# Kernel optimization log

Hardware: AMD Instinct MI355X
Metric: run time of the kernel (lower is better)

## Reference

```python
import jax, jax.numpy as jnp
import numpy as np
import math

DIM = 2048
B = 4
L = 4096
LOCAL_WINDOW = 512
GLOBAL_STRIDE = 1024
TOTAL_SEEN = 65536


def _sparse_cache_positions(total_seen):
    # Positions kept by _build_sparse_cache: local window tail + global strided.
    local_start = max(0, total_seen - LOCAL_WINDOW)
    glob = np.arange(0, local_start, GLOBAL_STRIDE)
    loc = np.arange(local_start, total_seen)
    return np.concatenate([glob, loc]).astype(np.int64)  # sorted, 576 entries


def setup_inputs() -> dict:
    key = jax.random.key(0)
    ks = jax.random.split(key, 12)
    pos = _sparse_cache_positions(TOTAL_SEEN)
    Kc = pos.shape[0]  # 576
    inp = {
        "chunk": jax.random.normal(ks[0], (B, L, DIM), dtype=jnp.float32),
        "cached_k": jax.random.normal(ks[1], (B, Kc, DIM), dtype=jnp.float32),
        "cached_v": jax.random.normal(ks[2], (B, Kc, DIM), dtype=jnp.float32),
        "cached_positions": jnp.asarray(pos),
        "total_seen": TOTAL_SEEN,
        "Wq": jax.random.normal(ks[3], (DIM, DIM), dtype=jnp.float32) * 0.02,
        "bq": jnp.zeros((DIM,), dtype=jnp.float32),
        "Wk": jax.random.normal(ks[4], (DIM, DIM), dtype=jnp.float32) * 0.02,
        "bk": jnp.zeros((DIM,), dtype=jnp.float32),
        "Wv": jax.random.normal(ks[5], (DIM, DIM), dtype=jnp.float32) * 0.02,
        "bv": jnp.zeros((DIM,), dtype=jnp.float32),
        "Wo": jax.random.normal(ks[6], (DIM, DIM), dtype=jnp.float32) * 0.02,
        "bo": jnp.zeros((DIM,), dtype=jnp.float32),
    }
    return inp


def reference(chunk, cached_k, cached_v, cached_positions, total_seen,
              Wq, bq, Wk, bk, Wv, bv, Wo, bo):
    Bn, Ln, D = chunk.shape
    scale = 1.0 / math.sqrt(D)
    # QKV projections (nn.Linear: x @ W.T + b)
    q = chunk @ Wq.T + bq            # [B, L, D]
    new_k = chunk @ Wk.T + bk        # [B, L, D]
    new_v = chunk @ Wv.T + bv
    new_pos = jnp.arange(total_seen, total_seen + Ln)  # [L]
    full_k = jnp.concatenate([cached_k, new_k], axis=1)   # [B, Kc+L, D]
    full_v = jnp.concatenate([cached_v, new_v], axis=1)
    full_pos = jnp.concatenate([cached_positions, new_pos], axis=0)  # [Kc+L]
    # Masked dense attention (causal on absolute positions)
    scores = jnp.einsum('bqd,bkd->bqk', q, full_k) * scale  # [B, L, Kc+L]
    causal = full_pos[None, :] > new_pos[:, None]           # [L, Kc+L]
    scores = jnp.where(causal[None, :, :], -jnp.inf, scores)
    weights = jax.nn.softmax(scores, axis=-1)
    attended = jnp.einsum('bqk,bkd->bqd', weights, full_v)  # [B, L, D]
    return attended @ Wo.T + bo
```

## Files before the change

kernel.cpp:

```cpp
#include <hip/hip_runtime.h>
#include <hip/hip_bf16.h>
#include <hip/hip_fp16.h>
#include <math.h>

#define B_   4
#define L_   4096
#define D_   2048
#define KC_  576
#define KT_  4672
#define KTP_ 4864

typedef __attribute__((ext_vector_type(8))) short short8;
typedef __attribute__((ext_vector_type(4))) float floatx4;

enum { EPI_BF16 = 0, EPI_KV = 1, EPI_SCORE = 2, EPI_F32 = 3 };
enum { FLAG_SWZ = 1, FLAG_KCAP = 2 };

__device__ static inline void gl_lds16(const void* g, void* l) {
  __builtin_amdgcn_global_load_lds((const __attribute__((address_space(1))) void*)g,
                                   (__attribute__((address_space(3))) void*)l,
                                   16, 0, 0);
}

__device__ static inline void barx() {
  asm volatile("" ::: "memory");
  __builtin_amdgcn_s_barrier();
  asm volatile("" ::: "memory");
}

__global__ __launch_bounds__(512, 2) void gemm_bt(
    const ushort* __restrict__ A, int lda,
    const ushort* __restrict__ Bt, int ldb,
    void* __restrict__ out, int ldo,
    const float* __restrict__ bias,
    int K, int mode, int flags, float scale)
{
  __shared__ __align__(16) char smem[2 * 4 * 16384];

  const int t = threadIdx.x;
  const int l = t & 63;
  const int wv = t >> 6;

  int m_idx, n_idx;
  if (flags & FLAG_SWZ) {
    const int total = gridDim.x * gridDim.y;
    const int chunk = total >> 3;
    const int orig = blockIdx.y * gridDim.x + blockIdx.x;
    const int wg = (orig & 7) * chunk + (orig >> 3);
    m_idx = wg % gridDim.y;
    n_idx = wg / gridDim.y;
  } else {
    n_idx = blockIdx.x;
    m_idx = blockIdx.y;
  }
  const int bm = m_idx * 256;
  const int bn = n_idx * 256;

  if (mode == EPI_SCORE && bn >= KC_ + bm + 256) return;
  if (flags & FLAG_KCAP) {
    const int kcap = 832 + 256 * m_idx;
    if (K > kcap) K = kcap;
  }

  const int wr = wv >> 2, wc = wv & 3;
  const int wm = wr << 7;
  const int wcn = wc << 6;
  const int fr = l & 15, fq = l >> 4;
  const int swz = fq ^ ((l >> 1) & 3);

  int offA[8], offB[4];
#pragma unroll
  for (int i = 0; i < 8; ++i) offA[i] = (wm + i * 16 + fr) * 64 + swz * 16;
#pragma unroll
  for (int j = 0; j < 4; ++j) offB[j] = (wcn + j * 16 + fr) * 64 + swz * 16;

  const int srow = t >> 2;
  const int sslot = (t & 3) ^ ((t >> 3) & 3);
  const ushort* Ag = A + (size_t)(bm + srow) * lda + sslot * 8;
  const ushort* Bg = Bt + (size_t)(bn + srow) * ldb + sslot * 8;
  const int wofs = wv << 10;

  auto stageA = [&](int d, int kh, int kt) {
    char* dst = smem + (((d << 2) + kh) << 14) + wofs;
    const ushort* g = Ag + kt + (kh << 5);
    gl_lds16(g, dst);
    gl_lds16(g + ((size_t)lda << 7), dst + 8192);
  };
  auto stageB = [&](int d, int kh, int kt) {
    char* dst = smem + (((d << 2) + 2 + kh) << 14) + wofs;
    const ushort* g = Bg + kt + (kh << 5);
    gl_lds16(g, dst);
    gl_lds16(g + ((size_t)ldb << 7), dst + 8192);
  };

  floatx4 acc[8][4];
#pragma unroll
  for (int i = 0; i < 8; ++i)
#pragma unroll
    for (int j = 0; j < 4; ++j) acc[i][j] = (floatx4)(0.0f);

  const int nkt = K >> 6;
  const int k1 = (nkt > 1) ? 64 : 0;

  stageA(0, 0, 0); stageB(0, 0, 0);
  stageA(0, 1, 0); stageB(0, 1, 0);
  stageA(1, 0, k1); stageB(1, 0, k1);
  asm volatile("s_waitcnt vmcnt(4)" ::: "memory");
  barx();

  for (int T = 0; T < nkt; ++T) {
    const int cur = T & 1;
    const char* rb = smem + (cur << 16);
    const int kA = ((T + 1 < nkt) ? T + 1 : nkt - 1) << 6;
    const int kB = ((T + 2 < nkt) ? T + 2 : nkt - 1) << 6;
    short8 afr[4], bfr[4];

#pragma unroll
    for (int i = 0; i < 4; ++i) afr[i] = *(const short8*)(rb + offA[i]);
#pragma unroll
    for (int j = 0; j < 4; ++j) bfr[j] = *(const short8*)(rb + 32768 + offB[j]);
    stageA(cur ^ 1, 1, kA);
    barx();
    __builtin_amdgcn_s_setprio(1);
#pragma unroll
    for (int i = 0; i < 4; ++i)
#pragma unroll
      for (int j = 0; j < 4; ++j)
        acc[i][j] = __builtin_amdgcn_mfma_f32_16x16x32_bf16(afr[i], bfr[j], acc[i][j], 0, 0, 0);
    __builtin_amdgcn_s_setprio(0);
    barx();

#pragma unroll
    for (int i = 0; i < 4; ++i) afr[i] = *(const short8*)(rb + offA[4 + i]);
    stageB(cur ^ 1, 1, kA);
    barx();
    __builtin_amdgcn_s_setprio(1);
#pragma unroll
    for (int i = 0; i < 4; ++i)
#pragma unroll
      for (int j = 0; j < 4; ++j)
        acc[4 + i][j] = __builtin_amdgcn_mfma_f32_16x16x32_bf16(afr[i], bfr[j], acc[4 + i][j], 0, 0, 0);
    __builtin_amdgcn_s_setprio(0);
    barx();

#pragma unroll
    for (int i = 0; i < 4; ++i) afr[i] = *(const short8*)(rb + 16384 + offA[i]);
#pragma unroll
    for (int j = 0; j < 4; ++j) bfr[j] = *(const short8*)(rb + 49152 + offB[j]);
    stageA(cur, 0, kB);
    barx();
    __builtin_amdgcn_s_setprio(1);
#pragma unroll
    for (int i = 0; i < 4; ++i)
#pragma unroll
      for (int j = 0; j < 4; ++j)
        acc[i][j] = __builtin_amdgcn_mfma_f32_16x16x32_bf16(afr[i], bfr[j], acc[i][j], 0, 0, 0);
    __builtin_amdgcn_s_setprio(0);
    barx();

#pragma unroll
    for (int i = 0; i < 4; ++i) afr[i] = *(const short8*)(rb + 16384 + offA[4 + i]);
    stageB(cur, 0, kB);
    asm volatile("s_waitcnt vmcnt(4)" ::: "memory");
    barx();
    __builtin_amdgcn_s_setprio(1);
#pragma unroll
    for (int i = 0; i < 4; ++i)
#pragma unroll
      for (int j = 0; j < 4; ++j)
        acc[4 + i][j] = __builtin_amdgcn_mfma_f32_16x16x32_bf16(afr[i], bfr[j], acc[4 + i][j], 0, 0, 0);
    __builtin_amdgcn_s_setprio(0);
    barx();
  }

#pragma unroll
  for (int mf = 0; mf < 8; ++mf) {
#pragma unroll
    for (int nf = 0; nf < 4; ++nf) {
      const int col = bn + wcn + nf * 16 + fr;
#pragma unroll
      for (int r = 0; r < 4; ++r) {
        const int row = bm + wm + mf * 16 + fq * 4 + r;
        float v = acc[mf][nf][r];
        if (mode == EPI_SCORE) {
          v *= scale;
          bool masked = (col >= KT_) || (col >= KC_ && (col - KC_) > row);
          if (masked) v = -65504.0f;
          ((__half*)out)[(size_t)row * ldo + col] = __float2half(v);
        } else if (mode == EPI_F32) {
          if (bias) v += bias[col];
          ((float*)out)[(size_t)row * ldo + col] = v;
        } else if (mode == EPI_KV) {
          if (bias) v += bias[col];
          const int b = row >> 12;
          const int ll = row & 4095;
          ((__hip_bfloat16*)out)[((size_t)b * KTP_ + KC_ + ll) * D_ + col] = __float2bfloat16(v);
        } else {
          if (bias) v += bias[col];
          ((__hip_bfloat16*)out)[(size_t)row * ldo + col] = __float2bfloat16(v);
        }
      }
    }
  }
}

__global__ __launch_bounds__(256) void cvt_f32_bf16(const float* __restrict__ in,
                                                    __hip_bfloat16* __restrict__ out, int n) {
  int i = blockIdx.x * 256 + threadIdx.x;
  int stride = gridDim.x * 256;
  for (; i < n; i += stride) out[i] = __float2bfloat16(in[i]);
}

__global__ __launch_bounds__(256) void cvt_weights(const float* __restrict__ wq,
                                                   const float* __restrict__ wk,
                                                   const float* __restrict__ wv,
                                                   const float* __restrict__ wo,
                                                   __hip_bfloat16* __restrict__ out) {
  const int per = D_ * D_;
  const int n = 4 * per;
  int i = blockIdx.x * 256 + threadIdx.x;
  int stride = gridDim.x * 256;
  for (; i < n; i += stride) {
    int w = i / per, rem = i - w * per;
    const float* src = (w == 0) ? wq : (w == 1) ? wk : (w == 2) ? wv : wo;
    out[i] = __float2bfloat16(src[rem]);
  }
}

__global__ __launch_bounds__(256) void cvt_cached(const float* __restrict__ ck,
                                                  const float* __restrict__ cv,
                                                  ushort* __restrict__ fk,
                                                  ushort* __restrict__ fv) {
  const int n = B_ * KC_ * D_;
  int i = blockIdx.x * 256 + threadIdx.x;
  int stride = gridDim.x * 256;
  for (; i < n; i += stride) {
    int b = i / (KC_ * D_);
    int rem = i - b * (KC_ * D_);
    size_t o = (size_t)b * KTP_ * D_ + rem;
    __hip_bfloat16 k16 = __float2bfloat16(ck[i]);
    __hip_bfloat16 v16 = __float2bfloat16(cv[i]);
    fk[o] = *(ushort*)&k16;
    fv[o] = *(ushort*)&v16;
  }
}

__global__ __launch_bounds__(256) void zero_pad(ushort* __restrict__ fk, ushort* __restrict__ fv) {
  const int n = B_ * (KTP_ - KT_) * D_;
  int i = blockIdx.x * 256 + threadIdx.x;
  int stride = gridDim.x * 256;
  for (; i < n; i += stride) {
    int b = i / ((KTP_ - KT_) * D_);
    int rem = i - b * ((KTP_ - KT_) * D_);
    size_t o = (size_t)b * KTP_ * D_ + (size_t)KT_ * D_ + rem;
    fk[o] = 0;
    fv[o] = 0;
  }
}

__global__ __launch_bounds__(256) void transpose_k(const ushort* __restrict__ in,
                                                   ushort* __restrict__ out) {
  __shared__ ushort tile[32][33];
  const int bx = blockIdx.x * 32;
  const int by = blockIdx.y * 32;
  const int t = threadIdx.x;
  for (int e = t; e < 1024; e += 256) {
    int r = e >> 5, c = e & 31;
    tile[r][c] = in[(size_t)(bx + r) * D_ + by + c];
  }
  __syncthreads();
  for (int e = t; e < 1024; e += 256) {
    int r = e >> 5, c = e & 31;
    out[(size_t)(by + r) * KTP_ + bx + c] = tile[c][r];
  }
}

__global__ __launch_bounds__(256) void softmax_rows(ushort* __restrict__ Sbuf) {
  const int row = blockIdx.x;
  const int nvalid = KC_ + row + 1;
  const int wcap = 832 + (row & ~255);
  ushort* sr = Sbuf + (size_t)row * KTP_;
  const int t = threadIdx.x;
  float vals[19];
  float m = -1e30f;
  int nit = (wcap - t + 255) / 256;
#pragma unroll
  for (int i = 0; i < 19; i++) {
    int idx = i * 256 + t;
    float v = -1e30f;
    if (idx < nvalid) v = __half2float(((const __half*)sr)[idx]);
    vals[i] = v;
    m = fmaxf(m, v);
    if (i + 1 >= nit) break;
  }
  __shared__ float red[256];
  red[t] = m;
  __syncthreads();
  for (int s = 128; s > 0; s >>= 1) {
    if (t < s) red[t] = fmaxf(red[t], red[t + s]);
    __syncthreads();
  }
  m = red[0];
  __syncthreads();
  float sum = 0.0f;
#pragma unroll
  for (int i = 0; i < 19; i++) {
    int idx = i * 256 + t;
    if (idx < wcap) {
      float e = (idx < nvalid) ? __expf(vals[i] - m) : 0.0f;
      vals[i] = e;
      sum += e;
    }
    if (i + 1 >= nit) break;
  }
  red[t] = sum;
  __syncthreads();
  for (int s = 128; s > 0; s >>= 1) {
    if (t < s) red[t] += red[t + s];
    __syncthreads();
  }
  float inv = 1.0f / red[0];
#pragma unroll
  for (int i = 0; i < 19; i++) {
    int idx = i * 256 + t;
    if (idx < wcap) {
      __hip_bfloat16 w = __float2bfloat16(vals[i] * inv);
      sr[idx] = *(ushort*)&w;
    }
    if (i + 1 >= nit) break;
  }
}

extern "C" void kernel_launch(void* const* d_in, const int* in_sizes, int n_in,
                              void* d_out, int out_size, void* d_ws, size_t ws_size,
                              hipStream_t stream) {
  const float* chunk    = (const float*)d_in[0];
  const float* cached_k = (const float*)d_in[1];
  const float* cached_v = (const float*)d_in[2];
  const float* Wq = (const float*)d_in[5];
  const float* bq = (const float*)d_in[6];
  const float* Wk = (const float*)d_in[7];
  const float* bk = (const float*)d_in[8];
  const float* Wv = (const float*)d_in[9];
  const float* bv = (const float*)d_in[10];
  const float* Wo = (const float*)d_in[11];
  const float* bo = (const float*)d_in[12];
  float* out = (float*)d_out;

  char* ws = (char*)d_ws;
  size_t off = 0;
  auto alloc = [&](size_t bytes) -> char* {
    char* p = ws + off;
    off += (bytes + 255) & ~(size_t)255;
    return p;
  };
  ushort* wall = (ushort*)alloc((size_t)4 * D_ * D_ * 2);
  ushort* wqb = wall;
  ushort* wkb = wall + (size_t)D_ * D_;
  ushort* wvb = wall + (size_t)2 * D_ * D_;
  ushort* wob = wall + (size_t)3 * D_ * D_;
  ushort* cbf = (ushort*)alloc((size_t)B_ * L_ * D_ * 2);
  ushort* qbf = (ushort*)alloc((size_t)B_ * L_ * D_ * 2);
  ushort* fk  = (ushort*)alloc((size_t)B_ * KTP_ * D_ * 2);
  ushort* fv  = (ushort*)alloc((size_t)B_ * KTP_ * D_ * 2);
  ushort* Sb  = (ushort*)alloc((size_t)L_ * KTP_ * 2);
  ushort* vt  = (ushort*)alloc((size_t)D_ * KTP_ * 2);

  dim3 blk(256);
  dim3 gblk(512);

  cvt_f32_bf16<<<8192, blk, 0, stream>>>(chunk, (__hip_bfloat16*)cbf, B_ * L_ * D_);
  cvt_weights<<<4096, blk, 0, stream>>>(Wq, Wk, Wv, Wo, (__hip_bfloat16*)wall);
  cvt_cached<<<2048, blk, 0, stream>>>(cached_k, cached_v, fk, fv);
  zero_pad<<<512, blk, 0, stream>>>(fk, fv);

  gemm_bt<<<dim3(D_ / 256, (B_ * L_) / 256), gblk, 0, stream>>>(
      cbf, D_, wqb, D_, qbf, D_, bq, D_, EPI_BF16, FLAG_SWZ, 1.0f);
  gemm_bt<<<dim3(D_ / 256, (B_ * L_) / 256), gblk, 0, stream>>>(
      cbf, D_, wkb, D_, fk, D_, bk, D_, EPI_KV, FLAG_SWZ, 1.0f);
  gemm_bt<<<dim3(D_ / 256, (B_ * L_) / 256), gblk, 0, stream>>>(
      cbf, D_, wvb, D_, fv, D_, bv, D_, EPI_KV, FLAG_SWZ, 1.0f);

  const float scale = 1.0f / sqrtf((float)D_);

  for (int b = 0; b < B_; b++) {
    const ushort* qb  = qbf + (size_t)b * L_ * D_;
    const ushort* fkb = fk  + (size_t)b * KTP_ * D_;
    const ushort* fvb = fv  + (size_t)b * KTP_ * D_;
    ushort* ab = cbf + (size_t)b * L_ * D_;

    transpose_k<<<dim3(KTP_ / 32, D_ / 32), blk, 0, stream>>>(fvb, vt);
    gemm_bt<<<dim3(KTP_ / 256, L_ / 256), gblk, 0, stream>>>(
        qb, D_, fkb, D_, Sb, KTP_, nullptr, D_, EPI_SCORE, FLAG_SWZ, scale);
    softmax_rows<<<L_, blk, 0, stream>>>(Sb);
    gemm_bt<<<dim3(D_ / 256, L_ / 256), gblk, 0, stream>>>(
        Sb, KTP_, vt, KTP_, ab, D_, nullptr, KT_, EPI_BF16, FLAG_SWZ | FLAG_KCAP, 1.0f);
  }

  gemm_bt<<<dim3(D_ / 256, (B_ * L_) / 256), gblk, 0, stream>>>(
      cbf, D_, wob, D_, out, D_, bo, D_, EPI_F32, FLAG_SWZ, 1.0f);
}
```

Measured before the change: 2.050 ms.

## Double-buffer GEMM fragment registers to prefetch LDS reads one phase ahead

Restructures the GEMM main loop so that LDS fragment loads for the next MFMA phase are issued before the current phase's MFMAs, using two register sets (a0/a1, b0/b1) in ping-pong. The next tile's first fragments are loaded at the end of each iteration, and a sched_barrier pins the schedule. An extra vmcnt wait is added before the third phase so the prefetched half-tile is resident. The aim is to hide LDS read latency behind MFMA work, at the cost of more VGPRs and possible occupancy or spill pressure. The global load address for the second half of each tile is also precomputed.

```diff
diff --git a/kernel.cpp b/kernel.cpp
--- a/kernel.cpp
+++ b/kernel.cpp
@@ -78,19 +78,19 @@
   const int sslot = (t & 3) ^ ((t >> 3) & 3);
   const ushort* Ag = A + (size_t)(bm + srow) * lda + sslot * 8;
   const ushort* Bg = Bt + (size_t)(bn + srow) * ldb + sslot * 8;
+  const ushort* AgH = Ag + ((size_t)lda << 7);
+  const ushort* BgH = Bg + ((size_t)ldb << 7);
   const int wofs = wv << 10;
 
   auto stageA = [&](int d, int kh, int kt) {
     char* dst = smem + (((d << 2) + kh) << 14) + wofs;
-    const ushort* g = Ag + kt + (kh << 5);
-    gl_lds16(g, dst);
-    gl_lds16(g + ((size_t)lda << 7), dst + 8192);
+    gl_lds16(Ag + kt + (kh << 5), dst);
+    gl_lds16(AgH + kt + (kh << 5), dst + 8192);
   };
   auto stageB = [&](int d, int kh, int kt) {
     char* dst = smem + (((d << 2) + 2 + kh) << 14) + wofs;
-    const ushort* g = Bg + kt + (kh << 5);
-    gl_lds16(g, dst);
-    gl_lds16(g + ((size_t)ldb << 7), dst + 8192);
+    gl_lds16(Bg + kt + (kh << 5), dst);
+    gl_lds16(BgH + kt + (kh << 5), dst + 8192);
   };
 
   floatx4 acc[8][4];
@@ -98,6 +98,21 @@
   for (int i = 0; i < 8; ++i)
 #pragma unroll
     for (int j = 0; j < 4; ++j) acc[i][j] = (floatx4)(0.0f);
+
+  auto mfma_lo = [&](short8 (&af)[4], short8 (&bf)[4]) {
+#pragma unroll
+    for (int i = 0; i < 4; ++i)
+#pragma unroll
+      for (int j = 0; j < 4; ++j)
+        acc[i][j] = __builtin_amdgcn_mfma_f32_16x16x32_bf16(af[i], bf[j], acc[i][j], 0, 0, 0);
+  };
+  auto mfma_hi = [&](short8 (&af)[4], short8 (&bf)[4]) {
+#pragma unroll
+    for (int i = 0; i < 4; ++i)
+#pragma unroll
+      for (int j = 0; j < 4; ++j)
+        acc[4 + i][j] = __builtin_amdgcn_mfma_f32_16x16x32_bf16(af[i], bf[j], acc[4 + i][j], 0, 0, 0);
+  };
 
   const int nkt = K >> 6;
   const int k1 = (nkt > 1) ? 64 : 0;
@@ -108,67 +123,62 @@
   asm volatile("s_waitcnt vmcnt(4)" ::: "memory");
   barx();
 
+  short8 a0[4], a1[4], b0[4], b1[4];
+#pragma unroll
+  for (int i = 0; i < 4; ++i) a0[i] = *(const short8*)(smem + offA[i]);
+#pragma unroll
+  for (int j = 0; j < 4; ++j) b0[j] = *(const short8*)(smem + 32768 + offB[j]);
+
   for (int T = 0; T < nkt; ++T) {
     const int cur = T & 1;
     const char* rb = smem + (cur << 16);
+    const char* rn = smem + ((cur ^ 1) << 16);
     const int kA = ((T + 1 < nkt) ? T + 1 : nkt - 1) << 6;
     const int kB = ((T + 2 < nkt) ? T + 2 : nkt - 1) << 6;
-    short8 afr[4], bfr[4];
-
-#pragma unroll
-    for (int i = 0; i < 4; ++i) afr[i] = *(const short8*)(rb + offA[i]);
-#pragma unroll
-    for (int j = 0; j < 4; ++j) bfr[j] = *(const short8*)(rb + 32768 + offB[j]);
+
+#pragma unroll
+    for (int i = 0; i < 4; ++i) a1[i] = *(const short8*)(rb + offA[4 + i]);
     stageA(cur ^ 1, 1, kA);
     barx();
+    __builtin_amdgcn_sched_barrier(0);
     __builtin_amdgcn_s_setprio(1);
-#pragma unroll
-    for (int i = 0; i < 4; ++i)
-#pragma unroll
-      for (int j = 0; j < 4; ++j)
-        acc[i][j] = __builtin_amdgcn_mfma_f32_16x16x32_bf16(afr[i], bfr[j], acc[i][j], 0, 0, 0);
+    mfma_lo(a0, b0);
     __builtin_amdgcn_s_setprio(0);
     barx();
 
 #pragma unroll
-    for (int i = 0; i < 4; ++i) afr[i] = *(const short8*)(rb + offA[4 + i]);
+    for (int i = 0; i < 4; ++i) a0[i] = *(const short8*)(rb + 16384 + offA[i]);
+#pragma unroll
+    for (int j = 0; j < 4; ++j) b1[j] = *(const short8*)(rb + 49152 + offB[j]);
     stageB(cur ^ 1, 1, kA);
     barx();
+    __builtin_amdgcn_sched_barrier(0);
     __builtin_amdgcn_s_setprio(1);
-#pragma unroll
-    for (int i = 0; i < 4; ++i)
-#pragma unroll
-      for (int j = 0; j < 4; ++j)
-        acc[4 + i][j] = __builtin_amdgcn_mfma_f32_16x16x32_bf16(afr[i], bfr[j], acc[4 + i][j], 0, 0, 0);
+    mfma_hi(a1, b0);
     __builtin_amdgcn_s_setprio(0);
     barx();
 
 #pragma unroll
-    for (int i = 0; i < 4; ++i) afr[i] = *(const short8*)(rb + 16384 + offA[i]);
-#pragma unroll
-    for (int j = 0; j < 4; ++j) bfr[j] = *(const short8*)(rb + 49152 + offB[j]);
+    for (int i = 0; i < 4; ++i) a1[i] = *(const short8*)(rb + 16384 + offA[4 + i]);
     stageA(cur, 0, kB);
-    barx();
+    asm volatile("s_waitcnt vmcnt(4)" ::: "memory");
+    barx();
+    __builtin_amdgcn_sched_barrier(0);
     __builtin_amdgcn_s_setprio(1);
-#pragma unroll
-    for (int i = 0; i < 4; ++i)
-#pragma unroll
-      for (int j = 0; j < 4; ++j)
-        acc[i][j] = __builtin_amdgcn_mfma_f32_16x16x32_bf16(afr[i], bfr[j], acc[i][j], 0, 0, 0);
+    mfma_lo(a0, b1);
     __builtin_amdgcn_s_setprio(0);
     barx();
 
 #pragma unroll
-    for (int i = 0; i < 4; ++i) afr[i] = *(const short8*)(rb + 16384 + offA[4 + i]);
+    for (int i = 0; i < 4; ++i) a0[i] = *(const short8*)(rn + offA[i]);
+#pragma unroll
+    for (int j = 0; j < 4; ++j) b0[j] = *(const short8*)(rn + 32768 + offB[j]);
     stageB(cur, 0, kB);
     asm volatile("s_waitcnt vmcnt(4)" ::: "memory");
     barx();
+    __builtin_amdgcn_sched_barrier(0);
     __builtin_amdgcn_s_setprio(1);
-#pragma unroll
-    for (int i = 0; i < 4; ++i)
-#pragma unroll
-      for (int j = 0; j < 4; ++j)
-        acc[4 + i][j] = __builtin_amdgcn_mfma_f32_16x16x32_bf16(afr[i], bfr[j], acc[4 + i][j], 0, 0, 0);
+    mfma_hi(a1, b1);
     __builtin_amdgcn_s_setprio(0);
     barx();
   }
```

New measurement: 2.074 ms. No clear change (+1.1%).
